# Performance work log

Hardware: AMD Instinct MI355X
Metric: run time of the kernel (lower is better)

The kernel has to match this reference:

```python
import jax, jax.numpy as jnp
import numpy as np


def conv1x1(x, W, b):
    # x: [B,C,H,W], W: [O,C], b: [O]  (torch Conv2d 1x1 squeezed)
    return jnp.einsum('oc,bchw->bohw', W, x) + b[None, :, None, None]


def setup_inputs() -> dict:
    key = jax.random.key(0)
    ks = jax.random.split(key, 7)
    B, C, H, W = 8, 256, 32, 32
    s = 1.0 / np.sqrt(C)
    x = jax.random.normal(ks[0], (B, C, H, W), jnp.float32)
    Wq = jax.random.normal(ks[1], (C, C), jnp.float32) * s
    bq = jax.random.normal(ks[2], (C,), jnp.float32) * 0.01
    Wk = jax.random.normal(ks[3], (C, C), jnp.float32) * s
    bk = jax.random.normal(ks[4], (C,), jnp.float32) * 0.01
    Wo = jax.random.normal(ks[5], (C, C), jnp.float32) * s
    bo = jax.random.normal(ks[6], (C,), jnp.float32) * 0.01
    return {"x": x, "Wq": Wq, "bq": bq, "Wk": Wk, "bk": bk, "Wo": Wo, "bo": bo}


def reference(x, Wq, bq, Wk, bk, Wo, bo):
    B, C, H, W = x.shape
    HW = H * W
    scale = 1.0 / (C ** 0.5)
    # proj_query: torch does view(B,C,HW).permute(0,2,1).transpose(1,2).contiguous().view(-1,C)
    # which is a row-major reshape of [B,C,HW] into [B*HW, C] (channel/spatial interleaved).
    # Reproduced faithfully.
    q = conv1x1(x, Wq, bq).reshape(B, C, HW).reshape(-1, C)          # [B*HW, C]
    # proj_key: view(B,C,HW).transpose(0,1).contiguous().view(C,-1) -> true [C, B*HW]
    k = jnp.transpose(conv1x1(x, Wk, bk).reshape(B, C, HW), (1, 0, 2)).reshape(C, -1)
    x_w = (q @ k).reshape(B * HW, B, HW)                              # [BHW, B, HW]
    out_co = jnp.max(x_w, axis=-1) + jnp.mean(x_w, axis=-1)           # [BHW, B]
    x_co = jnp.mean(out_co, axis=-1).reshape(B, HW) * scale           # [B, HW]
    x_co = jax.nn.softmax(x_co, axis=-1).reshape(B, 1, H, W)
    return conv1x1(x * x_co, Wo, bo)
```

## Files before the change

### kernel.cpp

```cpp
#include <hip/hip_runtime.h>

#define BATCH 8
#define CH 256
#define HWSZ 1024
#define BHW 8192

typedef _Float16 f16;
typedef _Float16 f16x4 __attribute__((ext_vector_type(4)));
typedef _Float16 f16x8 __attribute__((ext_vector_type(8)));
typedef float f32x4 __attribute__((ext_vector_type(4)));
typedef unsigned long long u64;
typedef __attribute__((address_space(3))) unsigned int lds_u32;
typedef __attribute__((address_space(1))) const unsigned int glob_u32;

__global__ __launch_bounds__(256) void kmeanW_kernel(
    const float* __restrict__ Wk, const float* __restrict__ bk,
    const float* __restrict__ xsum, float* __restrict__ kmean, float* __restrict__ ksum)
{
    __shared__ float xm[BATCH][CH];
    __shared__ float sm[32][8];
    const int tid = threadIdx.x;
#pragma unroll
    for (int i = 0; i < 8; ++i) xm[i][tid] = xsum[i * 256 + tid] * (1.0f / HWSZ);
    __syncthreads();

    const int co = blockIdx.x * 32 + (tid >> 3);
    const int b  = tid & 7;
    float acc = 0.f;
    const float4* w = (const float4*)(Wk + (size_t)co * CH);
    for (int c4 = 0; c4 < 64; ++c4) {
        float4 wv = w[c4];
        acc = fmaf(wv.x, xm[b][c4 * 4 + 0], acc);
        acc = fmaf(wv.y, xm[b][c4 * 4 + 1], acc);
        acc = fmaf(wv.z, xm[b][c4 * 4 + 2], acc);
        acc = fmaf(wv.w, xm[b][c4 * 4 + 3], acc);
    }
    const float v = acc + bk[co];
    kmean[b * 256 + co] = v;
    sm[tid >> 3][b] = v;
    __syncthreads();
    if (tid < 32) {
        float s = 0.f;
#pragma unroll
        for (int j = 0; j < 8; ++j) s += sm[tid][j];
        ksum[blockIdx.x * 32 + tid] = s;
    }
}

__global__ __launch_bounds__(256, 2) void pgemmQKY_kernel(
    const float* __restrict__ x,
    const float* __restrict__ Wq, const float* __restrict__ Wk, const float* __restrict__ Wo,
    const float* __restrict__ bq, const float* __restrict__ bk,
    f16* __restrict__ Qh, char* __restrict__ Ksw, f16* __restrict__ Yh,
    float* __restrict__ xsum)
{
    __shared__ __align__(16) char kbuf[32 * 1024];
    __shared__ __align__(16) float xt[256][36];
    f16* tile = (f16*)&xt[0][0];
    char* tileb = (char*)&xt[0][0];

    const int bid  = blockIdx.x;
    const int h    = bid >> 8;
    const int p    = bid & 255;
    const int pxg0 = p * 32;
    const int b    = pxg0 >> 10;
    const int hw0  = pxg0 & 1023;
    const int tid  = threadIdx.x;
    const int lane = tid & 63;
    const int wid  = tid >> 6;
    const int m = lane & 15, g = lane >> 4;
    const int coW = h * 128;

    {
        const int f4 = tid & 7;
        const int cs = tid >> 3;
#pragma unroll
        for (int pass = 0; pass < 8; ++pass) {
            const int c = pass * 32 + cs;
            float4 v = *(const float4*)(x + ((size_t)b * CH + c) * HWSZ + hw0 + f4 * 4);
            *(float4*)&xt[c][f4 * 4] = v;
        }
    }
    __syncthreads();

    {
        const int px = tid & 31;
        const int q8 = tid >> 5;
        const int sw = (px & 7) << 4;
#pragma unroll
        for (int r = 0; r < 4; ++r) {
            f16x8 hi, lo;
#pragma unroll
            for (int i = 0; i < 8; ++i) {
                const int c = q8 * 32 + r * 8 + i;
                float v = xt[c][px];
                f16 hv = (f16)v;
                hi[i] = hv;
                lo[i] = (f16)(v - (float)hv);
            }
            const int base = q8 * 64 + r * 16;
            *(f16x8*)(kbuf + px * 1024 + (base ^ sw)) = hi;
            *(f16x8*)(kbuf + px * 1024 + 512 + (base ^ sw)) = lo;
        }
    }

    if (h == 0) {
        float s = 0.f;
#pragma unroll
        for (int i4 = 0; i4 < 8; ++i4) {
            float4 v = *(const float4*)&xt[tid][i4 * 4];
            s += v.x + v.y + v.z + v.w;
        }
        atomicAdd(&xsum[b * 256 + tid], s);
    }

    f16x8 aA[2][8], aB[2][8];
#define LOAD_W(dst, Wsel)                                                                \
    {                                                                                    \
        _Pragma("unroll")                                                                \
        for (int t = 0; t < 2; ++t)                                                      \
            _Pragma("unroll")                                                            \
            for (int kk = 0; kk < 8; ++kk) {                                             \
                const float* wrow = (Wsel) + (size_t)(coW + wid * 32 + t * 16 + m) * CH + kk * 32 + g * 8; \
                float4 w0 = *(const float4*)(wrow);                                      \
                float4 w1 = *(const float4*)(wrow + 4);                                  \
                f16x8 av;                                                                \
                av[0] = (f16)w0.x; av[1] = (f16)w0.y; av[2] = (f16)w0.z; av[3] = (f16)w0.w; \
                av[4] = (f16)w1.x; av[5] = (f16)w1.y; av[6] = (f16)w1.z; av[7] = (f16)w1.w; \
                dst[t][kk] = av;                                                         \
            }                                                                            \
    }
    LOAD_W(aA, Wq);
    __syncthreads();

    const int sw0 = (m & 7) << 4;
    const f32x4 vz = {0.f, 0.f, 0.f, 0.f};
    f32x4 acc[2][2];

#define MFMA_PASS(ARR, NKS)                                                              \
    {                                                                                    \
        _Pragma("unroll")                                                                \
        for (int t = 0; t < 2; ++t) { acc[t][0] = vz; acc[t][1] = vz; }                  \
        _Pragma("unroll")                                                                \
        for (int ks = 0; ks < (NKS); ++ks) {                                             \
            const int X = ks * 64 + g * 16;                                              \
            f16x8 b0 = *(const f16x8*)(kbuf + m * 1024 + (X ^ sw0));                     \
            f16x8 b1 = *(const f16x8*)(kbuf + (16 + m) * 1024 + (X ^ sw0));              \
            _Pragma("unroll")                                                            \
            for (int t = 0; t < 2; ++t) {                                                \
                acc[t][0] = __builtin_amdgcn_mfma_f32_16x16x32_f16(ARR[t][ks & 7], b0, acc[t][0], 0, 0, 0); \
                acc[t][1] = __builtin_amdgcn_mfma_f32_16x16x32_f16(ARR[t][ks & 7], b1, acc[t][1], 0, 0, 0); \
            }                                                                            \
        }                                                                                \
    }

    MFMA_PASS(aA, 16);
    LOAD_W(aB, Wk);

#pragma unroll
    for (int t = 0; t < 2; ++t) {
        const int lco0 = wid * 32 + t * 16 + 4 * g;
        float4 bv = *(const float4*)(bq + coW + lco0);
        float ba[4] = {bv.x, bv.y, bv.z, bv.w};
#pragma unroll
        for (int u = 0; u < 2; ++u) {
            const int px = u * 16 + m;
#pragma unroll
            for (int j = 0; j < 4; ++j)
                tile[(lco0 + j) * 32 + (px ^ (j << 3))] = (f16)(acc[t][u][j] + ba[j]);
        }
    }
    __syncthreads();
#pragma unroll
    for (int pass = 0; pass < 2; ++pass) {
        const int lco = pass * 64 + (tid >> 2);
        const int run = tid & 3;
        f16x8 v = *(const f16x8*)(tile + lco * 32 + ((run * 8) ^ ((lco & 3) << 3)));
        *(f16x8*)(Qh + ((size_t)b * CH + coW + lco) * HWSZ + hw0 + run * 8) = v;
    }

    MFMA_PASS(aB, 16);
    LOAD_W(aA, Wo);
    __syncthreads();

#pragma unroll
    for (int t = 0; t < 2; ++t) {
        const int lco0 = wid * 32 + t * 16 + 4 * g;
        float4 bv = *(const float4*)(bk + coW + lco0);
        float ba[4] = {bv.x, bv.y, bv.z, bv.w};
#pragma unroll
        for (int u = 0; u < 2; ++u) {
            const int px = u * 16 + m;
            f16x4 pk;
#pragma unroll
            for (int j = 0; j < 4; ++j) pk[j] = (f16)(acc[t][u][j] + ba[j]);
            *(f16x4*)(tileb + px * 256 + ((lco0 * 2) ^ (m << 3))) = pk;
        }
    }
    __syncthreads();
    {
        const int px = tid & 31;
        const int rp = tid >> 5;
        const int kloc = (px & 15) << 3;
        const int kglb = (px & 7) << 4;
        char* grow = Ksw + (size_t)(pxg0 + px) * 512 + h * 256;
#pragma unroll
        for (int i = 0; i < 2; ++i) {
            const int rl = rp + i * 8;
            u64 a0 = *(const u64*)(tileb + px * 256 + ((rl * 16) ^ kloc));
            u64 a1 = *(const u64*)(tileb + px * 256 + ((rl * 16 + 8) ^ kloc));
            char* gdst = grow + ((rl * 16) ^ kglb);
            *(u64*)gdst = a0;
            *(u64*)(gdst + 8) = a1;
        }
    }

    MFMA_PASS(aA, 8);
    __syncthreads();

#pragma unroll
    for (int t = 0; t < 2; ++t) {
        const int lco0 = wid * 32 + t * 16 + 4 * g;
#pragma unroll
        for (int u = 0; u < 2; ++u) {
            const int px = u * 16 + m;
#pragma unroll
            for (int j = 0; j < 4; ++j)
                tile[(lco0 + j) * 32 + (px ^ (j << 3))] = (f16)acc[t][u][j];
        }
    }
    __syncthreads();
#pragma unroll
    for (int pass = 0; pass < 2; ++pass) {
        const int lco = pass * 64 + (tid >> 2);
        const int run = tid & 3;
        f16x8 v = *(const f16x8*)(tile + lco * 32 + ((run * 8) ^ ((lco & 3) << 3)));
        *(f16x8*)(Yh + ((size_t)b * CH + coW + lco) * HWSZ + hw0 + run * 8) = v;
    }
#undef MFMA_PASS
#undef LOAD_W
}

__global__ __launch_bounds__(256, 2) void score_kernel(
    const f16* __restrict__ Qh, const char* __restrict__ Ksw,
    const float* __restrict__ ksum, float* __restrict__ rowdq, float* __restrict__ rowq)
{
    __shared__ __align__(16) char kbuf[2][32768];
    __shared__ float lds_rm[128][2];
    __shared__ float lds_dq[128];
    __shared__ float kmS[CH];

    const int batch = blockIdx.x & 7;
    const int r0    = (blockIdx.x >> 3) * 128;
    const int tid   = threadIdx.x;
    const int lane  = tid & 63;
    const int wid   = tid >> 6;
    const int wr = wid >> 1, wc = wid & 1;
    const int m = lane & 15, g = lane >> 4;
    const int rbase = r0 + wr * 64;

    if (batch == 0) kmS[tid] = ksum[tid];

    const char* kbase = Ksw + (size_t)batch * HWSZ * 512;

#define STAGE(buf, ch)                                                                   \
    {                                                                                    \
        const char* _src = kbase + (ch) * 64 * 512 + tid * 16;                           \
        char* _dst = &kbuf[buf][tid * 16];                                               \
        _Pragma("unroll")                                                                \
        for (int k = 0; k < 8; ++k)                                                      \
            __builtin_amdgcn_global_load_lds((glob_u32*)(_src + k * 4096),               \
                                             (lds_u32*)(_dst + k * 4096), 16, 0, 0);     \
    }

    STAGE(0, 0);

    f16x8 a[4][8];
#pragma unroll
    for (int t = 0; t < 4; ++t)
#pragma unroll
        for (int kk = 0; kk < 8; ++kk)
            a[t][kk] = *(const f16x8*)(Qh + (size_t)(rbase + t * 16 + m) * CH + kk * 32 + 8 * g);
#pragma unroll
    for (int t = 0; t < 4; ++t)
#pragma unroll
        for (int kk = 0; kk < 8; ++kk)
            asm volatile("" : "+v"(a[t][kk]));

    int Ebase[2];
    {
        const int low = ((g * 16) ^ ((m & 3) << 4)) + (((m >> 2) & 1) << 6);
#pragma unroll
        for (int u2 = 0; u2 < 2; ++u2)
            Ebase[u2] = (wc * 32 + u2 * 16 + m) * 512 + low;
    }

    float rm[4][4];
#pragma unroll
    for (int t = 0; t < 4; ++t)
#pragma unroll
        for (int jj = 0; jj < 4; ++jj) rm[t][jj] = -1e30f;

    int cur = 0;
    for (int ch = 0; ch < 16; ++ch) {
        if (ch < 15) {
            STAGE(cur ^ 1, ch + 1);
            asm volatile("s_waitcnt vmcnt(8)" ::: "memory");
        } else {
            asm volatile("s_waitcnt vmcnt(0)" ::: "memory");
        }
        __builtin_amdgcn_s_barrier();

        const char* kb = &kbuf[cur][0];
        f32x4 acc[4][2];
        const f32x4 vz = {0.f, 0.f, 0.f, 0.f};
#pragma unroll
        for (int t = 0; t < 4; ++t) { acc[t][0] = vz; acc[t][1] = vz; }

#pragma unroll
        for (int kk = 0; kk < 8; ++kk) {
            f16x8 bfr[2];
            const int xorb = (kk & 1) << 6;
            const int imm  = (kk >> 1) * 128;
            bfr[0] = *(const f16x8*)(kb + (Ebase[0] ^ xorb) + imm);
            bfr[1] = *(const f16x8*)(kb + (Ebase[1] ^ xorb) + imm);
#pragma unroll
            for (int t = 0; t < 4; ++t) {
                acc[t][0] = __builtin_amdgcn_mfma_f32_16x16x32_f16(a[t][kk], bfr[0], acc[t][0], 0, 0, 0);
                acc[t][1] = __builtin_amdgcn_mfma_f32_16x16x32_f16(a[t][kk], bfr[1], acc[t][1], 0, 0, 0);
            }
        }

#pragma unroll
        for (int t = 0; t < 4; ++t)
#pragma unroll
            for (int jj = 0; jj < 4; ++jj)
                rm[t][jj] = fmaxf(rm[t][jj], fmaxf(acc[t][0][jj], acc[t][1][jj]));

        asm volatile("" ::: "memory");
        __builtin_amdgcn_s_barrier();
        cur ^= 1;
    }
#undef STAGE

#pragma unroll
    for (int d = 1; d < 16; d <<= 1)
#pragma unroll
        for (int t = 0; t < 4; ++t)
#pragma unroll
            for (int jj = 0; jj < 4; ++jj)
                rm[t][jj] = fmaxf(rm[t][jj], __shfl_xor(rm[t][jj], d, 64));

    if (m == 0) {
#pragma unroll
        for (int t = 0; t < 4; ++t)
#pragma unroll
            for (int jj = 0; jj < 4; ++jj)
                lds_rm[wr * 64 + t * 16 + g * 4 + jj][wc] = rm[t][jj];
    }

    if (batch == 0) {
        float dq[4];
#pragma unroll
        for (int t = 0; t < 4; ++t) {
            float s = 0.f;
#pragma unroll
            for (int kk = 0; kk < 8; ++kk)
#pragma unroll
                for (int i = 0; i < 8; ++i)
                    s = fmaf((float)a[t][kk][i], kmS[kk * 32 + 8 * g + i], s);
            s += __shfl_xor(s, 16, 64);
            s += __shfl_xor(s, 32, 64);
            dq[t] = s;
        }
        if (wc == 0 && lane < 16) {
#pragma unroll
            for (int t = 0; t < 4; ++t)
                lds_dq[wr * 64 + t * 16 + lane] = dq[t];
        }
        __syncthreads();
        if (tid < 128) {
            rowq[r0 + tid] = lds_dq[tid];
            rowdq[(size_t)(r0 + tid) * 8] = fmaxf(lds_rm[tid][0], lds_rm[tid][1]);
        }
    } else {
        __syncthreads();
        if (tid < 128)
            rowdq[(size_t)(r0 + tid) * 8 + batch] = fmaxf(lds_rm[tid][0], lds_rm[tid][1]);
    }
}

__global__ __launch_bounds__(256) void softmax_kernel(const float* __restrict__ rowdq,
                                                      const float* __restrict__ rowq,
                                                      float* __restrict__ wgt)
{
    const int br = blockIdx.x, tid = threadIdx.x;
    __shared__ float red[256];
    float l[4];
#pragma unroll
    for (int i = 0; i < 4; ++i) {
        const size_t r = (size_t)br * HWSZ + i * 256 + tid;
        float4 v0 = *(const float4*)(rowdq + r * 8);
        float4 v1 = *(const float4*)(rowdq + r * 8 + 4);
        l[i] = (v0.x + v0.y + v0.z + v0.w + v1.x + v1.y + v1.z + v1.w + rowq[r]) * (1.0f / 128.0f);
    }

    float mx = fmaxf(fmaxf(l[0], l[1]), fmaxf(l[2], l[3]));
    red[tid] = mx;
    __syncthreads();
    for (int s = 128; s > 0; s >>= 1) {
        if (tid < s) red[tid] = fmaxf(red[tid], red[tid + s]);
        __syncthreads();
    }
    mx = red[0];
    __syncthreads();

    float e[4], sm = 0.f;
#pragma unroll
    for (int i = 0; i < 4; ++i) { e[i] = expf(l[i] - mx); sm += e[i]; }
    red[tid] = sm;
    __syncthreads();
    for (int s = 128; s > 0; s >>= 1) {
        if (tid < s) red[tid] += red[tid + s];
        __syncthreads();
    }
    const float inv = 1.0f / red[0];
#pragma unroll
    for (int i = 0; i < 4; ++i)
        wgt[br * HWSZ + i * 256 + tid] = e[i] * inv;
}

__global__ __launch_bounds__(256) void gateY_kernel(const f16* __restrict__ Yh,
                                                    const float* __restrict__ wgt,
                                                    const float* __restrict__ bo,
                                                    float* __restrict__ out)
{
    const size_t idx = ((size_t)blockIdx.x * 256 + threadIdx.x) * 8;
    const int b  = (int)(idx >> 18);
    const int c  = (int)(idx >> 10) & 255;
    const int hw = (int)idx & 1023;

    f16x8 y = *(const f16x8*)(Yh + idx);
    float4 w0 = *(const float4*)(wgt + b * HWSZ + hw);
    float4 w1 = *(const float4*)(wgt + b * HWSZ + hw + 4);
    const float bov = bo[c];

    float4 o0, o1;
    o0.x = fmaf((float)y[0], w0.x, bov); o0.y = fmaf((float)y[1], w0.y, bov);
    o0.z = fmaf((float)y[2], w0.z, bov); o0.w = fmaf((float)y[3], w0.w, bov);
    o1.x = fmaf((float)y[4], w1.x, bov); o1.y = fmaf((float)y[5], w1.y, bov);
    o1.z = fmaf((float)y[6], w1.z, bov); o1.w = fmaf((float)y[7], w1.w, bov);
    *(float4*)(out + idx)     = o0;
    *(float4*)(out + idx + 4) = o1;
}

extern "C" void kernel_launch(void* const* d_in, const int* in_sizes, int n_in,
                              void* d_out, int out_size, void* d_ws, size_t ws_size,
                              hipStream_t stream)
{
    const float* x  = (const float*)d_in[0];
    const float* Wq = (const float*)d_in[1];
    const float* bq = (const float*)d_in[2];
    const float* Wk = (const float*)d_in[3];
    const float* bk = (const float*)d_in[4];
    const float* Wo = (const float*)d_in[5];
    const float* bo = (const float*)d_in[6];
    float* out = (float*)d_out;

    char* ws = (char*)d_ws;
    f16*   Qh     = (f16*)(ws);
    char*  Ksw    = (char*)(ws + (4 << 20));
    f16*   Yh     = (f16*)(ws + (8 << 20));
    float* xsum   = (float*)(ws + (12 << 20));
    float* rowdq  = (float*)(ws + (12 << 20) + (8 << 10));
    float* kmean  = (float*)(ws + (12 << 20) + (264 << 10));
    float* wgt    = (float*)(ws + (12 << 20) + (272 << 10));
    float* ksum   = (float*)(ws + (12 << 20) + (304 << 10));
    float* rowq   = (float*)(ws + (12 << 20) + (308 << 10));

    hipMemsetAsync(xsum, 0, 8 << 10, stream);

    pgemmQKY_kernel<<<dim3(512),  256, 0, stream>>>(x, Wq, Wk, Wo, bq, bk, Qh, Ksw, Yh, xsum);
    kmeanW_kernel  <<<dim3(8),    256, 0, stream>>>(Wk, bk, xsum, kmean, ksum);
    score_kernel   <<<dim3(512),  256, 0, stream>>>(Qh, Ksw, ksum, rowdq, rowq);
    softmax_kernel <<<dim3(8),    256, 0, stream>>>(rowdq, rowq, wgt);
    gateY_kernel   <<<dim3(1024), 256, 0, stream>>>(Yh, wgt, bo, out);
}
```

Measured before the change: 87.08 us.

## Fuse kmean into score kernel and softmax into gating, drop memset and atomics

Replaces the atomic xsum accumulation with per-block partial sums, so the memset is no longer needed. The small kmeanW kernel is folded into the batch-0 blocks of the score kernel, which now reduce the partials and compute the Wk·xmean term themselves. The softmax kernel is merged into the gating kernel, so each of the 1024 blocks recomputes its batch's softmax statistics. This cuts five launches plus a memset down to three, but adds redundant softmax reductions and expf work per block and puts a serial reduction on the batch-0 score blocks.

```diff
diff --git a/kernel.cpp b/kernel.cpp
--- a/kernel.cpp
+++ b/kernel.cpp
@@ -13,46 +13,12 @@
 typedef __attribute__((address_space(3))) unsigned int lds_u32;
 typedef __attribute__((address_space(1))) const unsigned int glob_u32;
 
-__global__ __launch_bounds__(256) void kmeanW_kernel(
-    const float* __restrict__ Wk, const float* __restrict__ bk,
-    const float* __restrict__ xsum, float* __restrict__ kmean, float* __restrict__ ksum)
-{
-    __shared__ float xm[BATCH][CH];
-    __shared__ float sm[32][8];
-    const int tid = threadIdx.x;
-#pragma unroll
-    for (int i = 0; i < 8; ++i) xm[i][tid] = xsum[i * 256 + tid] * (1.0f / HWSZ);
-    __syncthreads();
-
-    const int co = blockIdx.x * 32 + (tid >> 3);
-    const int b  = tid & 7;
-    float acc = 0.f;
-    const float4* w = (const float4*)(Wk + (size_t)co * CH);
-    for (int c4 = 0; c4 < 64; ++c4) {
-        float4 wv = w[c4];
-        acc = fmaf(wv.x, xm[b][c4 * 4 + 0], acc);
-        acc = fmaf(wv.y, xm[b][c4 * 4 + 1], acc);
-        acc = fmaf(wv.z, xm[b][c4 * 4 + 2], acc);
-        acc = fmaf(wv.w, xm[b][c4 * 4 + 3], acc);
-    }
-    const float v = acc + bk[co];
-    kmean[b * 256 + co] = v;
-    sm[tid >> 3][b] = v;
-    __syncthreads();
-    if (tid < 32) {
-        float s = 0.f;
-#pragma unroll
-        for (int j = 0; j < 8; ++j) s += sm[tid][j];
-        ksum[blockIdx.x * 32 + tid] = s;
-    }
-}
-
 __global__ __launch_bounds__(256, 2) void pgemmQKY_kernel(
     const float* __restrict__ x,
     const float* __restrict__ Wq, const float* __restrict__ Wk, const float* __restrict__ Wo,
     const float* __restrict__ bq, const float* __restrict__ bk,
     f16* __restrict__ Qh, char* __restrict__ Ksw, f16* __restrict__ Yh,
-    float* __restrict__ xsum)
+    float* __restrict__ xpartial)
 {
     __shared__ __align__(16) char kbuf[32 * 1024];
     __shared__ __align__(16) float xt[256][36];
@@ -111,7 +77,7 @@
             float4 v = *(const float4*)&xt[tid][i4 * 4];
             s += v.x + v.y + v.z + v.w;
         }
-        atomicAdd(&xsum[b * 256 + tid], s);
+        xpartial[p * 256 + tid] = s;
     }
 
     f16x8 aA[2][8], aB[2][8];
@@ -243,11 +209,14 @@
 
 __global__ __launch_bounds__(256, 2) void score_kernel(
     const f16* __restrict__ Qh, const char* __restrict__ Ksw,
-    const float* __restrict__ ksum, float* __restrict__ rowdq, float* __restrict__ rowq)
+    const float* __restrict__ Wk, const float* __restrict__ bk,
+    const float* __restrict__ xpartial,
+    float* __restrict__ rowdq, float* __restrict__ rowq)
 {
     __shared__ __align__(16) char kbuf[2][32768];
     __shared__ float lds_rm[128][2];
     __shared__ float lds_dq[128];
+    __shared__ float kmX[CH];
     __shared__ float kmS[CH];
 
     const int batch = blockIdx.x & 7;
@@ -259,8 +228,6 @@
     const int m = lane & 15, g = lane >> 4;
     const int rbase = r0 + wr * 64;
 
-    if (batch == 0) kmS[tid] = ksum[tid];
-
     const char* kbase = Ksw + (size_t)batch * HWSZ * 512;
 
 #define STAGE(buf, ch)                                                                   \
@@ -360,6 +327,28 @@
     }
 
     if (batch == 0) {
+        float xs[8] = {0.f, 0.f, 0.f, 0.f, 0.f, 0.f, 0.f, 0.f};
+        for (int pp = 0; pp < 32; ++pp) {
+#pragma unroll
+            for (int j = 0; j < 8; ++j)
+                xs[j] += xpartial[(pp * 8 + j) * 256 + tid];
+        }
+        float xstot = ((xs[0] + xs[1]) + (xs[2] + xs[3])) + ((xs[4] + xs[5]) + (xs[6] + xs[7]));
+        kmX[tid] = xstot * (1.0f / 1024.0f);
+        __syncthreads();
+
+        float accw = 0.f;
+        const float4* w = (const float4*)(Wk + (size_t)tid * CH);
+        for (int c4 = 0; c4 < 64; ++c4) {
+            float4 wv = w[c4];
+            accw = fmaf(wv.x, kmX[c4 * 4 + 0], accw);
+            accw = fmaf(wv.y, kmX[c4 * 4 + 1], accw);
+            accw = fmaf(wv.z, kmX[c4 * 4 + 2], accw);
+            accw = fmaf(wv.w, kmX[c4 * 4 + 3], accw);
+        }
+        kmS[tid] = accw + 8.0f * bk[tid];
+        __syncthreads();
+
         float dq[4];
 #pragma unroll
         for (int t = 0; t < 4; ++t) {
@@ -390,66 +379,63 @@
     }
 }
 
-__global__ __launch_bounds__(256) void softmax_kernel(const float* __restrict__ rowdq,
-                                                      const float* __restrict__ rowq,
-                                                      float* __restrict__ wgt)
+__global__ __launch_bounds__(256) void gateYS_kernel(const f16* __restrict__ Yh,
+                                                     const float* __restrict__ rowdq,
+                                                     const float* __restrict__ rowq,
+                                                     const float* __restrict__ bo,
+                                                     float* __restrict__ out)
 {
-    const int br = blockIdx.x, tid = threadIdx.x;
+    __shared__ float ld[HWSZ];
     __shared__ float red[256];
+
+    const int tid = threadIdx.x;
+    const size_t idx = ((size_t)blockIdx.x * 256 + tid) * 8;
+    const int b  = (int)(idx >> 18);
+    const int c  = (int)(idx >> 10) & 255;
+    const int hw = (int)idx & 1023;
+
     float l[4];
+    float lmax = -1e30f;
 #pragma unroll
     for (int i = 0; i < 4; ++i) {
-        const size_t r = (size_t)br * HWSZ + i * 256 + tid;
+        const size_t r = (size_t)b * HWSZ + i * 256 + tid;
         float4 v0 = *(const float4*)(rowdq + r * 8);
         float4 v1 = *(const float4*)(rowdq + r * 8 + 4);
         l[i] = (v0.x + v0.y + v0.z + v0.w + v1.x + v1.y + v1.z + v1.w + rowq[r]) * (1.0f / 128.0f);
-    }
-
-    float mx = fmaxf(fmaxf(l[0], l[1]), fmaxf(l[2], l[3]));
-    red[tid] = mx;
+        ld[i * 256 + tid] = l[i];
+        lmax = fmaxf(lmax, l[i]);
+    }
+    red[tid] = lmax;
     __syncthreads();
     for (int s = 128; s > 0; s >>= 1) {
         if (tid < s) red[tid] = fmaxf(red[tid], red[tid + s]);
         __syncthreads();
     }
-    mx = red[0];
-    __syncthreads();
-
-    float e[4], sm = 0.f;
-#pragma unroll
-    for (int i = 0; i < 4; ++i) { e[i] = expf(l[i] - mx); sm += e[i]; }
-    red[tid] = sm;
+    const float mx = red[0];
+    __syncthreads();
+
+    float es = 0.f;
+#pragma unroll
+    for (int i = 0; i < 4; ++i) es += expf(l[i] - mx);
+    red[tid] = es;
     __syncthreads();
     for (int s = 128; s > 0; s >>= 1) {
         if (tid < s) red[tid] += red[tid + s];
         __syncthreads();
     }
     const float inv = 1.0f / red[0];
-#pragma unroll
-    for (int i = 0; i < 4; ++i)
-        wgt[br * HWSZ + i * 256 + tid] = e[i] * inv;
-}
-
-__global__ __launch_bounds__(256) void gateY_kernel(const f16* __restrict__ Yh,
-                                                    const float* __restrict__ wgt,
-                                                    const float* __restrict__ bo,
-                                                    float* __restrict__ out)
-{
-    const size_t idx = ((size_t)blockIdx.x * 256 + threadIdx.x) * 8;
-    const int b  = (int)(idx >> 18);
-    const int c  = (int)(idx >> 10) & 255;
-    const int hw = (int)idx & 1023;
 
     f16x8 y = *(const f16x8*)(Yh + idx);
-    float4 w0 = *(const float4*)(wgt + b * HWSZ + hw);
-    float4 w1 = *(const float4*)(wgt + b * HWSZ + hw + 4);
     const float bov = bo[c];
-
     float4 o0, o1;
-    o0.x = fmaf((float)y[0], w0.x, bov); o0.y = fmaf((float)y[1], w0.y, bov);
-    o0.z = fmaf((float)y[2], w0.z, bov); o0.w = fmaf((float)y[3], w0.w, bov);
-    o1.x = fmaf((float)y[4], w1.x, bov); o1.y = fmaf((float)y[5], w1.y, bov);
-    o1.z = fmaf((float)y[6], w1.z, bov); o1.w = fmaf((float)y[7], w1.w, bov);
+    o0.x = fmaf((float)y[0], expf(ld[hw + 0] - mx) * inv, bov);
+    o0.y = fmaf((float)y[1], expf(ld[hw + 1] - mx) * inv, bov);
+    o0.z = fmaf((float)y[2], expf(ld[hw + 2] - mx) * inv, bov);
+    o0.w = fmaf((float)y[3], expf(ld[hw + 3] - mx) * inv, bov);
+    o1.x = fmaf((float)y[4], expf(ld[hw + 4] - mx) * inv, bov);
+    o1.y = fmaf((float)y[5], expf(ld[hw + 5] - mx) * inv, bov);
+    o1.z = fmaf((float)y[6], expf(ld[hw + 6] - mx) * inv, bov);
+    o1.w = fmaf((float)y[7], expf(ld[hw + 7] - mx) * inv, bov);
     *(float4*)(out + idx)     = o0;
     *(float4*)(out + idx + 4) = o1;
 }
@@ -468,21 +454,14 @@
     float* out = (float*)d_out;
 
     char* ws = (char*)d_ws;
-    f16*   Qh     = (f16*)(ws);
-    char*  Ksw    = (char*)(ws + (4 << 20));
-    f16*   Yh     = (f16*)(ws + (8 << 20));
-    float* xsum   = (float*)(ws + (12 << 20));
-    float* rowdq  = (float*)(ws + (12 << 20) + (8 << 10));
-    float* kmean  = (float*)(ws + (12 << 20) + (264 << 10));
-    float* wgt    = (float*)(ws + (12 << 20) + (272 << 10));
-    float* ksum   = (float*)(ws + (12 << 20) + (304 << 10));
-    float* rowq   = (float*)(ws + (12 << 20) + (308 << 10));
-
-    hipMemsetAsync(xsum, 0, 8 << 10, stream);
-
-    pgemmQKY_kernel<<<dim3(512),  256, 0, stream>>>(x, Wq, Wk, Wo, bq, bk, Qh, Ksw, Yh, xsum);
-    kmeanW_kernel  <<<dim3(8),    256, 0, stream>>>(Wk, bk, xsum, kmean, ksum);
-    score_kernel   <<<dim3(512),  256, 0, stream>>>(Qh, Ksw, ksum, rowdq, rowq);
-    softmax_kernel <<<dim3(8),    256, 0, stream>>>(rowdq, rowq, wgt);
-    gateY_kernel   <<<dim3(1024), 256, 0, stream>>>(Yh, wgt, bo, out);
+    f16*   Qh       = (f16*)(ws);
+    char*  Ksw      = (char*)(ws + (4 << 20));
+    f16*   Yh       = (f16*)(ws + (8 << 20));
+    float* xpartial = (float*)(ws + (12 << 20));
+    float* rowdq    = (float*)(ws + (12 << 20) + (256 << 10));
+    float* rowq     = (float*)(ws + (12 << 20) + (512 << 10));
+
+    pgemmQKY_kernel<<<dim3(512),  256, 0, stream>>>(x, Wq, Wk, Wo, bq, bk, Qh, Ksw, Yh, xpartial);
+    score_kernel   <<<dim3(512),  256, 0, stream>>>(Qh, Ksw, Wk, bk, xpartial, rowdq, rowq);
+    gateYS_kernel  <<<dim3(1024), 256, 0, stream>>>(Yh, rowdq, rowq, bo, out);
 }
```

New measurement: 93.21 us. 7.0% more time.
